# Performance work log

Measured on AMD Instinct MI355X. Metric: run time of the kernel, lower is better.

Reference implementation:

```python
import jax, jax.numpy as jnp
import numpy as np

N_HEADS = 16
N_EMBED = 1024
HEAD_DIM = N_EMBED // N_HEADS
B, T = 4, 2048


def setup_inputs() -> dict:
    key = jax.random.key(0)
    k1, k2, k3 = jax.random.split(key, 3)
    scale = 1.0 / np.sqrt(N_EMBED)
    x = jax.random.normal(k1, (B, T, N_EMBED), dtype=jnp.float32)
    w_qkv = jax.random.normal(k2, (N_EMBED, 3 * N_EMBED), dtype=jnp.float32) * scale
    w_out = jax.random.normal(k3, (N_EMBED, N_EMBED), dtype=jnp.float32) * scale
    b_out = jnp.zeros((N_EMBED,), dtype=jnp.float32)
    return {"x": x, "w_qkv": w_qkv, "w_out": w_out, "b_out": b_out}


def reference(x, w_qkv, w_out, b_out):
    b, t, c = x.shape
    # qkv projection (no bias), split into q,k,v per head: [B, H, T, D]
    qkv = (x @ w_qkv).reshape(b, t, 3, N_HEADS, HEAD_DIM)
    q, k, v = jnp.moveaxis(qkv, 2, 0)            # each [B, T, H, D]
    q = jnp.swapaxes(q, 1, 2) * (HEAD_DIM ** -0.5)  # [B, H, T, D]
    k = jnp.swapaxes(k, 1, 2)
    v = jnpp = jnp.swapaxes(v, 1, 2)
    # scores + causal mask
    attn = jnp.einsum('bhqd,bhkd->bhqk', q, k)   # [B, H, T, T]
    causal = jnp.tril(jnp.ones((t, t), dtype=bool))
    attn = jnp.where(causal, attn, -jnp.inf)
    attn = jax.nn.softmax(attn, axis=-1)
    out = jnp.einsum('bhqk,bhkd->bhqd', attn, v)  # [B, H, T, D]
    out = jnp.swapaxes(out, 1, 2).reshape(b, t, c)
    # output projection (dropout is identity in eval mode)
    return out @ w_out + b_out
```

## Files before the change

kernel.cpp:

```cpp
#include <hip/hip_runtime.h>

#define NH 16
#define HD 64
#define CE 1024
#define TT 2048
#define BB 4
#define MM 8192

using bf16x8 = __attribute__((ext_vector_type(8))) __bf16;
using f32x4  = __attribute__((ext_vector_type(4))) float;

__device__ __forceinline__ unsigned short f2bf(float f) {
  unsigned int u = __float_as_uint(f);
  u += 0x7fffu + ((u >> 16) & 1u);
  return (unsigned short)(u >> 16);
}
__device__ __forceinline__ unsigned short f2bf_rtz(float f) {
  return (unsigned short)(__float_as_uint(f) >> 16);
}

__device__ __forceinline__ void async_cp16(const unsigned short* g, unsigned short* l) {
  __builtin_amdgcn_global_load_lds(
      (const __attribute__((address_space(1))) unsigned int*)g,
      (__attribute__((address_space(3))) unsigned int*)l, 16, 0, 0);
}

__global__ __launch_bounds__(256) void convert_x(const float* __restrict__ in,
                                                 unsigned short* __restrict__ out) {
  const int i = (blockIdx.x * 256 + threadIdx.x) * 4;
  const float4 v = *(const float4*)(in + i);
  ushort4 o;
  o.x = f2bf(v.x); o.y = f2bf(v.y); o.z = f2bf(v.z); o.w = f2bf(v.w);
  *(ushort4*)(out + i) = o;
}

__global__ __launch_bounds__(256) void transpose_conv(const float* __restrict__ in,
                                                      unsigned short* __restrict__ out,
                                                      int rows, int cols) {
  __shared__ unsigned short tile[32][33];
  int c0 = blockIdx.x * 32, r0 = blockIdx.y * 32;
  int tx = threadIdx.x & 31, ty = threadIdx.x >> 5;
#pragma unroll
  for (int i = ty; i < 32; i += 8)
    tile[i][tx] = f2bf(in[(size_t)(r0 + i) * cols + c0 + tx]);
  __syncthreads();
#pragma unroll
  for (int i = ty; i < 32; i += 8)
    out[(size_t)(c0 + i) * rows + r0 + tx] = tile[tx][i];
}

__global__ __launch_bounds__(256) void transpose_v(const unsigned short* __restrict__ in,
                                                   unsigned short* __restrict__ out) {
  __shared__ unsigned short tile[32][33];
  const int bh = blockIdx.z;
  const int t0 = blockIdx.y * 32, d0 = blockIdx.x * 32;
  const int tx = threadIdx.x & 31, ty = threadIdx.x >> 5;
  const size_t base = (size_t)bh * TT * HD;
#pragma unroll
  for (int i = ty; i < 32; i += 8)
    tile[i][tx] = in[base + (size_t)(t0 + i) * HD + d0 + tx];
  __syncthreads();
#pragma unroll
  for (int i = ty; i < 32; i += 8)
    out[base + (size_t)(d0 + i) * TT + t0 + tx] = tile[tx][i];
}

__device__ __forceinline__ void gemm_core(const unsigned short* __restrict__ A,
                                          const unsigned short* __restrict__ BT,
                                          int m0, int n0, f32x4 (&acc)[4][4]) {
  __shared__ unsigned short As[128 * 32];
  __shared__ unsigned short Bs[128 * 32];
  const int tid  = threadIdx.x;
  const int lane = tid & 63;
  const int wave = tid >> 6;
  const int quad = lane >> 4;
  const int l15  = lane & 15;
  const int wm = (wave & 1) * 64;
  const int wn = (wave >> 1) * 64;
  const int ldr = tid >> 2;
  const int ldc = (tid & 3) * 8;
  const unsigned short* Ap = A + (size_t)(m0 + ldr) * CE + ldc;
  const unsigned short* Bp = BT + (size_t)(n0 + ldr) * CE + ldc;
  unsigned short* AsW0 = As + wave * 512;
  unsigned short* AsW1 = As + 2048 + wave * 512;
  unsigned short* BsW0 = Bs + wave * 512;
  unsigned short* BsW1 = Bs + 2048 + wave * 512;
  for (int k0 = 0; k0 < CE; k0 += 32) {
    async_cp16(Ap + k0, AsW0);
    async_cp16(Ap + (size_t)64 * CE + k0, AsW1);
    async_cp16(Bp + k0, BsW0);
    async_cp16(Bp + (size_t)64 * CE + k0, BsW1);
    __syncthreads();
    bf16x8 af[4], bfr[4];
#pragma unroll
    for (int i = 0; i < 4; i++) {
      af[i]  = *(const bf16x8*)&As[(wm + i * 16 + l15) * 32 + quad * 8];
      bfr[i] = *(const bf16x8*)&Bs[(wn + i * 16 + l15) * 32 + quad * 8];
    }
#pragma unroll
    for (int mi = 0; mi < 4; mi++)
#pragma unroll
      for (int ni = 0; ni < 4; ni++)
        acc[mi][ni] = __builtin_amdgcn_mfma_f32_16x16x32_bf16(af[mi], bfr[ni], acc[mi][ni], 0, 0, 0);
    __syncthreads();
  }
}

__global__ __launch_bounds__(256) void gemm_qkv(const unsigned short* __restrict__ A,
                                                const unsigned short* __restrict__ BT,
                                                unsigned short* __restrict__ Qb,
                                                unsigned short* __restrict__ Kb,
                                                unsigned short* __restrict__ Vb) {
  f32x4 acc[4][4] = {};
  const int m0 = blockIdx.y * 128, n0 = blockIdx.x * 128;
  gemm_core(A, BT, m0, n0, acc);
  const int tid = threadIdx.x, lane = tid & 63, wave = tid >> 6;
  const int quad = lane >> 4, l15 = lane & 15;
  const int wm = (wave & 1) * 64, wn = (wave >> 1) * 64;
  const float QSCALE = 0.125f * 1.44269504088896340736f;
#pragma unroll
  for (int mi = 0; mi < 4; mi++) {
#pragma unroll
    for (int ni = 0; ni < 4; ni++) {
      const int n = n0 + wn + ni * 16 + l15;
      const int s = n >> 10;
      const int h = (n >> 6) & 15;
      const int d = n & 63;
#pragma unroll
      for (int r = 0; r < 4; r++) {
        const int m = m0 + wm + mi * 16 + quad * 4 + r;
        const int b = m >> 11;
        const int t = m & 2047;
        const int bh = (b << 4) + h;
        const float v = acc[mi][ni][r];
        if (s == 0)      Qb[((size_t)bh * TT + t) * HD + d] = f2bf(v * QSCALE);
        else if (s == 1) Kb[((size_t)bh * TT + t) * HD + d] = f2bf(v);
        else             Vb[((size_t)bh * TT + t) * HD + d] = f2bf(v);
      }
    }
  }
}

__global__ __launch_bounds__(256) void gemm_out(const unsigned short* __restrict__ A,
                                                const unsigned short* __restrict__ BT,
                                                const float* __restrict__ bias,
                                                float* __restrict__ out) {
  f32x4 acc[4][4] = {};
  const int m0 = blockIdx.y * 128, n0 = blockIdx.x * 128;
  gemm_core(A, BT, m0, n0, acc);
  const int tid = threadIdx.x, lane = tid & 63, wave = tid >> 6;
  const int quad = lane >> 4, l15 = lane & 15;
  const int wm = (wave & 1) * 64, wn = (wave >> 1) * 64;
#pragma unroll
  for (int mi = 0; mi < 4; mi++) {
#pragma unroll
    for (int ni = 0; ni < 4; ni++) {
      const int n = n0 + wn + ni * 16 + l15;
      const float bv = bias[n];
#pragma unroll
      for (int r = 0; r < 4; r++) {
        const int m = m0 + wm + mi * 16 + quad * 4 + r;
        out[(size_t)m * CE + n] = acc[mi][ni][r] + bv;
      }
    }
  }
}

__global__ __launch_bounds__(512) void flash_attn(const unsigned short* __restrict__ Q,
                                                  const unsigned short* __restrict__ Kg,
                                                  const unsigned short* __restrict__ Vt,
                                                  unsigned short* __restrict__ AO) {
  __shared__ unsigned short Ks[64][72];
  __shared__ unsigned short Vs[64][72];
  __shared__ unsigned short Ps[8][16][72];
  const int flat = blockIdx.x + 8 * blockIdx.y;
  const int wu   = (flat & 7) * 64 + (flat >> 3);
  const int qx   = wu & 7;
  const int bh   = wu >> 3;
  const int tid = threadIdx.x, w = tid >> 6, lane = tid & 63;
  const int quad = lane >> 4, l15 = lane & 15;
  const int b = bh >> 4, h = bh & 15;
  const unsigned short* Kbase = Kg + (size_t)bh * TT * HD;
  const unsigned short* Vbase = Vt + (size_t)bh * HD * TT;
  const int srow = tid >> 3;
  const int scol = (tid & 7) * 8;
  const bf16x8 ones = {1, 1, 1, 1, 1, 1, 1, 1};

  for (int ph = 0; ph < 2; ph++) {
    const int pt = ph ? (15 - qx) : qx;
    const int q0 = pt * 128;
    const int n_it = 2 * pt + 2;
    const int rbase = q0 + w * 16;
    bf16x8 qf[2];
    {
      const unsigned short* Qp =
          Q + ((size_t)bh * TT + rbase + l15) * HD + quad * 8;
      qf[0] = *(const bf16x8*)Qp;
      qf[1] = *(const bf16x8*)(Qp + 32);
    }
    f32x4 o[4] = {};
    f32x4 l_acc = {};
    uint4 kreg, vreg;
    {
      kreg = *(const uint4*)(Kbase + (size_t)srow * HD + scol);
      vreg = *(const uint4*)(Vbase + (size_t)srow * TT + scol);
    }
    for (int it = 0; it < n_it; it++) {
      const int kv0 = it * 64;
      *(uint4*)&Ks[srow][scol] = kreg;
      *(uint4*)&Vs[srow][scol] = vreg;
      {
        const int itn = (it + 1 < n_it) ? it + 1 : it;
        const int kvn = itn * 64;
        kreg = *(const uint4*)(Kbase + (size_t)(kvn + srow) * HD + scol);
        vreg = *(const uint4*)(Vbase + (size_t)srow * TT + kvn + scol);
      }
      __syncthreads();
      if (kv0 <= rbase + 15) {
        bf16x8 kb[4][2];
#pragma unroll
        for (int ni = 0; ni < 4; ni++) {
          kb[ni][0] = *(const bf16x8*)&Ks[ni * 16 + l15][quad * 8];
          kb[ni][1] = *(const bf16x8*)&Ks[ni * 16 + l15][32 + quad * 8];
        }
        f32x4 s[4];
        __builtin_amdgcn_s_setprio(1);
#pragma unroll
        for (int ni = 0; ni < 4; ni++) {
          f32x4 z = {};
          z = __builtin_amdgcn_mfma_f32_16x16x32_bf16(qf[0], kb[ni][0], z, 0, 0, 0);
          z = __builtin_amdgcn_mfma_f32_16x16x32_bf16(qf[1], kb[ni][1], z, 0, 0, 0);
          s[ni] = z;
        }
        __builtin_amdgcn_s_setprio(0);
        if (kv0 + 63 > rbase) {
#pragma unroll
          for (int ni = 0; ni < 4; ni++) {
            const int col_g = kv0 + ni * 16 + l15;
#pragma unroll
            for (int r = 0; r < 4; r++) {
              const int row_g = rbase + quad * 4 + r;
              const float sv = (col_g <= row_g) ? s[ni][r] : -1e30f;
              Ps[w][quad * 4 + r][ni * 16 + l15] = f2bf_rtz(exp2f(sv));
            }
          }
        } else {
#pragma unroll
          for (int ni = 0; ni < 4; ni++)
#pragma unroll
            for (int r = 0; r < 4; r++)
              Ps[w][quad * 4 + r][ni * 16 + l15] = f2bf_rtz(exp2f(s[ni][r]));
        }
        bf16x8 pa[2];
        pa[0] = *(const bf16x8*)&Ps[w][l15][quad * 8];
        pa[1] = *(const bf16x8*)&Ps[w][l15][32 + quad * 8];
        bf16x8 vb[4][2];
#pragma unroll
        for (int nd = 0; nd < 4; nd++) {
          vb[nd][0] = *(const bf16x8*)&Vs[nd * 16 + l15][quad * 8];
          vb[nd][1] = *(const bf16x8*)&Vs[nd * 16 + l15][32 + quad * 8];
        }
        __builtin_amdgcn_s_setprio(1);
        l_acc = __builtin_amdgcn_mfma_f32_16x16x32_bf16(pa[0], ones, l_acc, 0, 0, 0);
        l_acc = __builtin_amdgcn_mfma_f32_16x16x32_bf16(pa[1], ones, l_acc, 0, 0, 0);
#pragma unroll
        for (int nd = 0; nd < 4; nd++) {
          o[nd] = __builtin_amdgcn_mfma_f32_16x16x32_bf16(pa[0], vb[nd][0], o[nd], 0, 0, 0);
          o[nd] = __builtin_amdgcn_mfma_f32_16x16x32_bf16(pa[1], vb[nd][1], o[nd], 0, 0, 0);
        }
        __builtin_amdgcn_s_setprio(0);
      }
      __syncthreads();
    }
    {
      float rin[4];
#pragma unroll
      for (int r = 0; r < 4; r++) rin[r] = __builtin_amdgcn_rcpf(l_acc[r]);
#pragma unroll
      for (int nd = 0; nd < 4; nd++)
#pragma unroll
        for (int r = 0; r < 4; r++) {
          const int row_g = rbase + quad * 4 + r;
          const size_t mg = (size_t)b * TT + row_g;
          AO[mg * CE + h * 64 + nd * 16 + l15] = f2bf(o[nd][r] * rin[r]);
        }
    }
  }
}

extern "C" void kernel_launch(void* const* d_in, const int* in_sizes, int n_in,
                              void* d_out, int out_size, void* d_ws, size_t ws_size,
                              hipStream_t stream) {
  const float* x     = (const float*)d_in[0];
  const float* w_qkv = (const float*)d_in[1];
  const float* w_out = (const float*)d_in[2];
  const float* b_out = (const float*)d_in[3];
  float* out = (float*)d_out;

  unsigned short* ws  = (unsigned short*)d_ws;
  unsigned short* Xb  = ws;
  unsigned short* Wt1 = Xb  + (size_t)MM * CE;
  unsigned short* Wt2 = Wt1 + (size_t)3072 * 1024;
  unsigned short* Qb  = Wt2 + (size_t)1024 * 1024;
  unsigned short* Kb  = Qb  + (size_t)8388608;
  unsigned short* Vb  = Kb  + (size_t)8388608;
  unsigned short* Vtb = Vb  + (size_t)8388608;
  unsigned short* AO  = Vtb + (size_t)8388608;

  convert_x     <<<dim3(8192), 256, 0, stream>>>(x, Xb);
  transpose_conv<<<dim3(96, 32), 256, 0, stream>>>(w_qkv, Wt1, 1024, 3072);
  transpose_conv<<<dim3(32, 32), 256, 0, stream>>>(w_out, Wt2, 1024, 1024);
  gemm_qkv  <<<dim3(24, 64), 256, 0, stream>>>(Xb, Wt1, Qb, Kb, Vb);
  transpose_v<<<dim3(2, 64, 64), 256, 0, stream>>>(Vb, Vtb);
  flash_attn<<<dim3(8, 64), 512, 0, stream>>>(Qb, Kb, Vtb, AO);
  gemm_out  <<<dim3(8, 64), 256, 0, stream>>>(AO, Wt2, b_out, out);
}
```

Baseline: 274.9 us.

## Load K fragments straight to registers and double-buffer V in LDS

The flash-attention loop no longer stages K through shared memory. Each wave loads its K MFMA fragments directly from global memory into registers and prefetches the next tile's fragments after the QK MFMAs. V now uses a double-buffered LDS tile, which removes one of the two __syncthreads per iteration. LDS row padding changes from 72 to 74 elements. The trade-off is that each of the 8 waves now fetches the full K tile from global memory (more L2 traffic), and the 148-byte row stride may break 16-byte alignment for the vector LDS accesses.

```diff
diff --git a/kernel.cpp b/kernel.cpp
--- a/kernel.cpp
+++ b/kernel.cpp
@@ -170,9 +170,8 @@
                                                   const unsigned short* __restrict__ Kg,
                                                   const unsigned short* __restrict__ Vt,
                                                   unsigned short* __restrict__ AO) {
-  __shared__ unsigned short Ks[64][72];
-  __shared__ unsigned short Vs[64][72];
-  __shared__ unsigned short Ps[8][16][72];
+  __shared__ unsigned short Vs[2][64][74];
+  __shared__ unsigned short Ps[8][16][74];
   const int flat = blockIdx.x + 8 * blockIdx.y;
   const int wu   = (flat & 7) * 64 + (flat >> 3);
   const int qx   = wu & 7;
@@ -200,29 +199,26 @@
     }
     f32x4 o[4] = {};
     f32x4 l_acc = {};
-    uint4 kreg, vreg;
-    {
-      kreg = *(const uint4*)(Kbase + (size_t)srow * HD + scol);
-      vreg = *(const uint4*)(Vbase + (size_t)srow * TT + scol);
-    }
+    const unsigned short* Kf = Kbase + (size_t)l15 * HD + quad * 8;
+    uint4 vreg = *(const uint4*)(Vbase + (size_t)srow * TT + scol);
+    *(uint4*)&Vs[0][srow][scol] = vreg;
+    bf16x8 kb[4][2];
+#pragma unroll
+    for (int ni = 0; ni < 4; ni++) {
+      kb[ni][0] = *(const bf16x8*)(Kf + (size_t)(ni * 16) * HD);
+      kb[ni][1] = *(const bf16x8*)(Kf + (size_t)(ni * 16) * HD + 32);
+    }
+    vreg = *(const uint4*)(Vbase + (size_t)srow * TT + (n_it > 1 ? 64 : 0) + scol);
+    __syncthreads();
     for (int it = 0; it < n_it; it++) {
       const int kv0 = it * 64;
-      *(uint4*)&Ks[srow][scol] = kreg;
-      *(uint4*)&Vs[srow][scol] = vreg;
-      {
-        const int itn = (it + 1 < n_it) ? it + 1 : it;
-        const int kvn = itn * 64;
-        kreg = *(const uint4*)(Kbase + (size_t)(kvn + srow) * HD + scol);
-        vreg = *(const uint4*)(Vbase + (size_t)srow * TT + kvn + scol);
+      const int cur = it & 1;
+      if (it + 1 < n_it) {
+        *(uint4*)&Vs[cur ^ 1][srow][scol] = vreg;
+        const int itn = (it + 2 < n_it) ? it + 2 : it + 1;
+        vreg = *(const uint4*)(Vbase + (size_t)srow * TT + itn * 64 + scol);
       }
-      __syncthreads();
       if (kv0 <= rbase + 15) {
-        bf16x8 kb[4][2];
-#pragma unroll
-        for (int ni = 0; ni < 4; ni++) {
-          kb[ni][0] = *(const bf16x8*)&Ks[ni * 16 + l15][quad * 8];
-          kb[ni][1] = *(const bf16x8*)&Ks[ni * 16 + l15][32 + quad * 8];
-        }
         f32x4 s[4];
         __builtin_amdgcn_s_setprio(1);
 #pragma unroll
@@ -233,6 +229,14 @@
           s[ni] = z;
         }
         __builtin_amdgcn_s_setprio(0);
+        if ((it + 1 < n_it) && (kv0 + 64 <= rbase + 15)) {
+          const unsigned short* Kn = Kf + (size_t)(kv0 + 64) * HD;
+#pragma unroll
+          for (int ni = 0; ni < 4; ni++) {
+            kb[ni][0] = *(const bf16x8*)(Kn + (size_t)(ni * 16) * HD);
+            kb[ni][1] = *(const bf16x8*)(Kn + (size_t)(ni * 16) * HD + 32);
+          }
+        }
         if (kv0 + 63 > rbase) {
 #pragma unroll
           for (int ni = 0; ni < 4; ni++) {
@@ -257,8 +261,8 @@
         bf16x8 vb[4][2];
 #pragma unroll
         for (int nd = 0; nd < 4; nd++) {
-          vb[nd][0] = *(const bf16x8*)&Vs[nd * 16 + l15][quad * 8];
-          vb[nd][1] = *(const bf16x8*)&Vs[nd * 16 + l15][32 + quad * 8];
+          vb[nd][0] = *(const bf16x8*)&Vs[cur][nd * 16 + l15][quad * 8];
+          vb[nd][1] = *(const bf16x8*)&Vs[cur][nd * 16 + l15][32 + quad * 8];
         }
         __builtin_amdgcn_s_setprio(1);
         l_acc = __builtin_amdgcn_mfma_f32_16x16x32_bf16(pa[0], ones, l_acc, 0, 0, 0);
```

New measurement: 331.4 us. 1.21x slower.

## Merge prep kernels and fuse V transpose into QKV GEMM epilogue

Applied to the files above, without the earlier changes.

Combines the x conversion and the two weight transpose-convert kernels into one launch that dispatches on block index. The QKV GEMM blocks that produce V now transpose their tile through shared memory and write V directly in [B,H,D,T] layout, so the separate transpose_v kernel and the intermediate V buffer go away. This removes two launches and one full read and write of V, at the cost of extra LDS traffic and barriers in the V-producing GEMM blocks.

```diff
diff --git a/kernel.cpp b/kernel.cpp
--- a/kernel.cpp
+++ b/kernel.cpp
@@ -25,21 +25,36 @@
       (__attribute__((address_space(3))) unsigned int*)l, 16, 0, 0);
 }
 
-__global__ __launch_bounds__(256) void convert_x(const float* __restrict__ in,
-                                                 unsigned short* __restrict__ out) {
-  const int i = (blockIdx.x * 256 + threadIdx.x) * 4;
-  const float4 v = *(const float4*)(in + i);
-  ushort4 o;
-  o.x = f2bf(v.x); o.y = f2bf(v.y); o.z = f2bf(v.z); o.w = f2bf(v.w);
-  *(ushort4*)(out + i) = o;
-}
-
-__global__ __launch_bounds__(256) void transpose_conv(const float* __restrict__ in,
-                                                      unsigned short* __restrict__ out,
-                                                      int rows, int cols) {
+__global__ __launch_bounds__(256) void prep(const float* __restrict__ x,
+                                            const float* __restrict__ w_qkv,
+                                            const float* __restrict__ w_out,
+                                            unsigned short* __restrict__ Xb,
+                                            unsigned short* __restrict__ Wt1,
+                                            unsigned short* __restrict__ Wt2) {
   __shared__ unsigned short tile[32][33];
-  int c0 = blockIdx.x * 32, r0 = blockIdx.y * 32;
-  int tx = threadIdx.x & 31, ty = threadIdx.x >> 5;
+  const int idx = blockIdx.x;
+  if (idx < 8192) {
+    const int i = (idx * 256 + threadIdx.x) * 4;
+    const float4 v = *(const float4*)(x + i);
+    ushort4 o;
+    o.x = f2bf(v.x); o.y = f2bf(v.y); o.z = f2bf(v.z); o.w = f2bf(v.w);
+    *(ushort4*)(Xb + i) = o;
+    return;
+  }
+  const float* in;
+  unsigned short* out;
+  int rows, cols, bx, by;
+  if (idx < 11264) {
+    const int tc = idx - 8192;
+    in = w_qkv; out = Wt1; rows = 1024; cols = 3072;
+    bx = tc % 96; by = tc / 96;
+  } else {
+    const int tc = idx - 11264;
+    in = w_out; out = Wt2; rows = 1024; cols = 1024;
+    bx = tc & 31; by = tc >> 5;
+  }
+  const int c0 = bx * 32, r0 = by * 32;
+  const int tx = threadIdx.x & 31, ty = threadIdx.x >> 5;
 #pragma unroll
   for (int i = ty; i < 32; i += 8)
     tile[i][tx] = f2bf(in[(size_t)(r0 + i) * cols + c0 + tx]);
@@ -49,27 +64,10 @@
     out[(size_t)(c0 + i) * rows + r0 + tx] = tile[tx][i];
 }
 
-__global__ __launch_bounds__(256) void transpose_v(const unsigned short* __restrict__ in,
-                                                   unsigned short* __restrict__ out) {
-  __shared__ unsigned short tile[32][33];
-  const int bh = blockIdx.z;
-  const int t0 = blockIdx.y * 32, d0 = blockIdx.x * 32;
-  const int tx = threadIdx.x & 31, ty = threadIdx.x >> 5;
-  const size_t base = (size_t)bh * TT * HD;
-#pragma unroll
-  for (int i = ty; i < 32; i += 8)
-    tile[i][tx] = in[base + (size_t)(t0 + i) * HD + d0 + tx];
-  __syncthreads();
-#pragma unroll
-  for (int i = ty; i < 32; i += 8)
-    out[base + (size_t)(d0 + i) * TT + t0 + tx] = tile[tx][i];
-}
-
 __device__ __forceinline__ void gemm_core(const unsigned short* __restrict__ A,
                                           const unsigned short* __restrict__ BT,
-                                          int m0, int n0, f32x4 (&acc)[4][4]) {
-  __shared__ unsigned short As[128 * 32];
-  __shared__ unsigned short Bs[128 * 32];
+                                          int m0, int n0, f32x4 (&acc)[4][4],
+                                          unsigned short* As, unsigned short* Bs) {
   const int tid  = threadIdx.x;
   const int lane = tid & 63;
   const int wave = tid >> 6;
@@ -110,13 +108,48 @@
                                                 const unsigned short* __restrict__ BT,
                                                 unsigned short* __restrict__ Qb,
                                                 unsigned short* __restrict__ Kb,
-                                                unsigned short* __restrict__ Vb) {
+                                                unsigned short* __restrict__ Vtb) {
+  __shared__ unsigned short pool[8448];
   f32x4 acc[4][4] = {};
   const int m0 = blockIdx.y * 128, n0 = blockIdx.x * 128;
-  gemm_core(A, BT, m0, n0, acc);
+  gemm_core(A, BT, m0, n0, acc, pool, pool + 4096);
   const int tid = threadIdx.x, lane = tid & 63, wave = tid >> 6;
   const int quad = lane >> 4, l15 = lane & 15;
   const int wm = (wave & 1) * 64, wn = (wave >> 1) * 64;
+  if (blockIdx.x >= 16) {
+    unsigned short* Vt = pool;
+    const int h0 = 2 * (blockIdx.x - 16);
+    const int bb = m0 >> 11;
+    const int t0g = m0 & 2047;
+    const int l31 = tid & 31;
+    const int rw  = tid >> 5;
+    unsigned int* __restrict__ VtU = (unsigned int*)Vtb;
+#pragma unroll
+    for (int hp = 0; hp < 2; hp++) {
+      __syncthreads();
+      if ((wave & 1) == hp) {
+#pragma unroll
+        for (int mi = 0; mi < 4; mi++)
+#pragma unroll
+          for (int ni = 0; ni < 4; ni++) {
+            const int row = wn + ni * 16 + l15;
+            const int col = mi * 16 + quad * 4;
+#pragma unroll
+            for (int r = 0; r < 4; r++)
+              Vt[row * 66 + col + r] = f2bf(acc[mi][ni][r]);
+          }
+      }
+      __syncthreads();
+#pragma unroll
+      for (int k = 0; k < 16; k++) {
+        const int d = rw + 8 * k;
+        const unsigned int v = *(const unsigned int*)&Vt[d * 66 + 2 * l31];
+        const int hh = h0 + (d >> 6);
+        VtU[((((size_t)(bb * 16 + hh) * 64 + (d & 63)) * TT + t0g + 64 * hp) >> 1) + l31] = v;
+      }
+    }
+    return;
+  }
   const float QSCALE = 0.125f * 1.44269504088896340736f;
 #pragma unroll
   for (int mi = 0; mi < 4; mi++) {
@@ -133,9 +166,8 @@
         const int t = m & 2047;
         const int bh = (b << 4) + h;
         const float v = acc[mi][ni][r];
-        if (s == 0)      Qb[((size_t)bh * TT + t) * HD + d] = f2bf(v * QSCALE);
-        else if (s == 1) Kb[((size_t)bh * TT + t) * HD + d] = f2bf(v);
-        else             Vb[((size_t)bh * TT + t) * HD + d] = f2bf(v);
+        if (s == 0) Qb[((size_t)bh * TT + t) * HD + d] = f2bf(v * QSCALE);
+        else        Kb[((size_t)bh * TT + t) * HD + d] = f2bf(v);
       }
     }
   }
@@ -145,9 +177,10 @@
                                                 const unsigned short* __restrict__ BT,
                                                 const float* __restrict__ bias,
                                                 float* __restrict__ out) {
+  __shared__ unsigned short pool[8192];
   f32x4 acc[4][4] = {};
   const int m0 = blockIdx.y * 128, n0 = blockIdx.x * 128;
-  gemm_core(A, BT, m0, n0, acc);
+  gemm_core(A, BT, m0, n0, acc, pool, pool + 4096);
   const int tid = threadIdx.x, lane = tid & 63, wave = tid >> 6;
   const int quad = lane >> 4, l15 = lane & 15;
   const int wm = (wave & 1) * 64, wn = (wave >> 1) * 64;
@@ -303,15 +336,11 @@
   unsigned short* Wt2 = Wt1 + (size_t)3072 * 1024;
   unsigned short* Qb  = Wt2 + (size_t)1024 * 1024;
   unsigned short* Kb  = Qb  + (size_t)8388608;
-  unsigned short* Vb  = Kb  + (size_t)8388608;
-  unsigned short* Vtb = Vb  + (size_t)8388608;
+  unsigned short* Vtb = Kb  + (size_t)8388608;
   unsigned short* AO  = Vtb + (size_t)8388608;
 
-  convert_x     <<<dim3(8192), 256, 0, stream>>>(x, Xb);
-  transpose_conv<<<dim3(96, 32), 256, 0, stream>>>(w_qkv, Wt1, 1024, 3072);
-  transpose_conv<<<dim3(32, 32), 256, 0, stream>>>(w_out, Wt2, 1024, 1024);
-  gemm_qkv  <<<dim3(24, 64), 256, 0, stream>>>(Xb, Wt1, Qb, Kb, Vb);
-  transpose_v<<<dim3(2, 64, 64), 256, 0, stream>>>(Vb, Vtb);
+  prep      <<<dim3(12288), 256, 0, stream>>>(x, w_qkv, w_out, Xb, Wt1, Wt2);
+  gemm_qkv  <<<dim3(24, 64), 256, 0, stream>>>(Xb, Wt1, Qb, Kb, Vtb);
   flash_attn<<<dim3(8, 64), 512, 0, stream>>>(Qb, Kb, Vtb, AO);
   gemm_out  <<<dim3(8, 64), 256, 0, stream>>>(AO, Wt2, b_out, out);
 }
```

New measurement: 263.6 us. 1.04x faster.
